# Kernel optimization log

Measured on AMD Instinct MI355X. Metric: run time of the kernel, lower is better.

The kernel has to match this reference:

```python
import jax, jax.numpy as jnp
import numpy as np

N_EMBD = 1024
N_HEAD = 16

def setup_inputs() -> dict:
    key = jax.random.key(0)
    k1, k2, k3 = jax.random.split(key, 3)
    x = jax.random.normal(k1, (2, 2048, N_EMBD), dtype=jnp.float32)
    # torch Linear(n, 3n): y = x @ W_attn (we store transposed weight directly)
    w_attn = jax.random.normal(k2, (N_EMBD, 3 * N_EMBD), dtype=jnp.float32) * 0.02
    w_proj = jax.random.normal(k3, (N_EMBD, N_EMBD), dtype=jnp.float32) * 0.02
    return {"x": x, "w_attn": w_attn, "w_proj": w_proj}

def reference(x, w_attn, w_proj):
    B, S, E = x.shape
    H = N_HEAD
    D = E // H
    qkv = x @ w_attn  # [B, S, 3E]
    q, k, v = jnp.split(qkv, 3, axis=-1)
    # [B, H, S, D]
    q = q.reshape(B, S, H, D).transpose(0, 2, 1, 3)
    k = k.reshape(B, S, H, D).transpose(0, 2, 1, 3)
    v = v.reshape(B, S, H, D).transpose(0, 2, 1, 3)
    scale = 1.0 / jnp.sqrt(jnp.asarray(D, dtype=x.dtype))
    a = jnp.einsum('bhqd,bhkd->bhqk', q, k) * scale  # [B, H, S, S]
    causal = jnp.tril(jnp.ones((S, S), dtype=bool))
    a = jnp.where(causal, a, -jnp.inf)
    a = jax.nn.softmax(a, axis=-1)
    y = jnp.einsum('bhqk,bhkd->bhqd', a, v)  # [B, H, S, D]
    y = y.transpose(0, 2, 1, 3).reshape(B, S, E)
    return y @ w_proj
```

## Files before the change

kernel.cpp:

```cpp
#include <hip/hip_runtime.h>

#define DEVI __device__ __forceinline__

typedef short bf16x8 __attribute__((ext_vector_type(8)));
typedef float f32x4 __attribute__((ext_vector_type(4)));
typedef unsigned short u16;
typedef unsigned int u32;

static constexpr int Bn = 2, S = 2048, E = 1024, H = 16, D = 64;
static constexpr int Mrows = Bn * S;
static constexpr int N_QKV = 3 * E;

DEVI u16 f2b(float f) {
  union { float f; u32 u; } c; c.f = f;
  return (u16)((c.u + 0x7FFFu + ((c.u >> 16) & 1u)) >> 16);
}

DEVI bf16x8 ld8(const u16* p) {
  union { uint4 u; bf16x8 v; } c;
  c.u = *reinterpret_cast<const uint4*>(p);
  return c.v;
}

#define MFMA(a, b, c) __builtin_amdgcn_mfma_f32_16x16x32_bf16(a, b, c, 0, 0, 0)

#define G2L16(gptr, lptr) \
  __builtin_amdgcn_global_load_lds((const __attribute__((address_space(1))) void*)(gptr), \
                                   (__attribute__((address_space(3))) void*)(lptr), 16, 0, 0)

__global__ void conv_bf16(const float* __restrict__ in, u16* __restrict__ out, int n4) {
  int i = blockIdx.x * blockDim.x + threadIdx.x;
  if (i < n4) {
    float4 f = reinterpret_cast<const float4*>(in)[i];
    ushort4 u;
    u.x = f2b(f.x); u.y = f2b(f.y); u.z = f2b(f.z); u.w = f2b(f.w);
    reinterpret_cast<ushort4*>(out)[i] = u;
  }
}

__global__ void transpose_bf16(const float* __restrict__ in, u16* __restrict__ out, int R, int C) {
  __shared__ float t[32][33];
  int bx = blockIdx.x * 32;
  int by = blockIdx.y * 32;
  int tx = threadIdx.x, ty = threadIdx.y;
#pragma unroll
  for (int k = 0; k < 32; k += 8)
    t[ty + k][tx] = in[(size_t)(by + ty + k) * C + bx + tx];
  __syncthreads();
#pragma unroll
  for (int k = 0; k < 32; k += 8)
    out[(size_t)(bx + ty + k) * R + by + tx] = f2b(t[tx][ty + k]);
}

__global__ __launch_bounds__(256) void gemm_qkv(const u16* __restrict__ A, const u16* __restrict__ BT,
                                                u16* __restrict__ Qb, u16* __restrict__ Kb,
                                                u16* __restrict__ VbT) {
  constexpr int K = 1024, BK = 64;
  __shared__ __align__(16) u16 As[128 * BK];
  __shared__ __align__(16) u16 Bs[128 * BK];
  int tid = threadIdx.x;
  int w = tid >> 6, lane = tid & 63, quad = lane >> 4, l15 = lane & 15;
  int m0 = blockIdx.x * 128, n0 = blockIdx.y * 128;
  int mw = (w >> 1) * 64, nw = (w & 1) * 64;
  const u16* Ab = A + (size_t)m0 * K;
  const u16* Bb = BT + (size_t)n0 * K;
  f32x4 acc[4][4] = {};
  for (int k0 = 0; k0 < K; k0 += BK) {
#pragma unroll
    for (int j = 0; j < 4; j++) {
      int L = j * 256 + tid;
      int row = L >> 3, cg = (L & 7) ^ (row & 7);
      G2L16(Ab + (size_t)row * K + k0 + cg * 8, (char*)As + L * 16);
    }
#pragma unroll
    for (int j = 0; j < 4; j++) {
      int L = j * 256 + tid;
      int row = L >> 3, cg = (L & 7) ^ (row & 7);
      G2L16(Bb + (size_t)row * K + k0 + cg * 8, (char*)Bs + L * 16);
    }
    __syncthreads();
#pragma unroll
    for (int kk = 0; kk < 2; kk++) {
      int sg = ((kk << 2) | quad) ^ (l15 & 7);
      bf16x8 a[4], b[4];
#pragma unroll
      for (int i = 0; i < 4; i++) a[i] = ld8(&As[(mw + i * 16 + l15) * BK + sg * 8]);
#pragma unroll
      for (int i = 0; i < 4; i++) b[i] = ld8(&Bs[(nw + i * 16 + l15) * BK + sg * 8]);
#pragma unroll
      for (int mb = 0; mb < 4; mb++)
#pragma unroll
        for (int nb = 0; nb < 4; nb++)
          acc[mb][nb] = MFMA(a[mb], b[nb], acc[mb][nb]);
    }
    __syncthreads();
  }
#pragma unroll
  for (int mb = 0; mb < 4; mb++) {
    int m = m0 + mw + mb * 16 + quad * 4;
    int b = m >> 11, s = m & 2047;
#pragma unroll
    for (int nb = 0; nb < 4; nb++) {
      int n = n0 + nw + nb * 16 + l15;
      int sec = n >> 10, e = n & 1023, h = e >> 6, d = e & 63;
      int bh = b * H + h;
      if (sec == 0) {
#pragma unroll
        for (int r = 0; r < 4; r++)
          Qb[((size_t)bh * S + s + r) * D + d] = f2b(acc[mb][nb][r] * 0.125f);
      } else if (sec == 1) {
#pragma unroll
        for (int r = 0; r < 4; r++)
          Kb[((size_t)bh * S + s + r) * D + d] = f2b(acc[mb][nb][r]);
      } else {
        ushort4 v;
        v.x = f2b(acc[mb][nb][0]); v.y = f2b(acc[mb][nb][1]);
        v.z = f2b(acc[mb][nb][2]); v.w = f2b(acc[mb][nb][3]);
        *reinterpret_cast<ushort4*>(VbT + ((size_t)bh * D + d) * S + s) = v;
      }
    }
  }
}

__global__ __launch_bounds__(256, 3) void attn(const u16* __restrict__ Qb, const u16* __restrict__ Kb,
                                               const u16* __restrict__ VbT, u16* __restrict__ Yb) {
  __shared__ __align__(16) u16 Ks[128 * 64];
  __shared__ __align__(16) u16 Vs[64 * 128];
  __shared__ __align__(16) u32 Ps[4][16 * 68];
  int w = threadIdx.x >> 6, lane = threadIdx.x & 63, quad = lane >> 4, l15 = lane & 15;
  int bh = blockIdx.x & 31, p = blockIdx.x >> 5;
  int b = bh >> 4, h = bh & 15;
  int qtA = 31 - p, qtB = p;
  int ncA = (qtA + 2) >> 1, ncB = (qtB + 2) >> 1;

  const u16* Kbh = Kb + (size_t)bh * S * D;
  const u16* Vbh = VbT + (size_t)bh * D * S;
  u32* myP = &Ps[w][0];
  const u16* myP16 = (const u16*)myP;
  int prow = l15 * 68 + quad * 2;

  int qbA = qtA * 64 + w * 16, qbB = qtB * 64 + w * 16;
  int kmaxA = qbA + 16, kmaxB = qbB + 16;
  const u16* QpA = Qb + ((size_t)bh * S + qbA + l15) * D + quad * 8;
  const u16* QpB = Qb + ((size_t)bh * S + qbB + l15) * D + quad * 8;
  bf16x8 bqA0 = ld8(QpA), bqA1 = ld8(QpA + 32);
  bf16x8 bqB0 = ld8(QpB), bqB1 = ld8(QpB + 32);

  float lA = 0.f, lB = 0.f;
  f32x4 oA[4] = {}, oB[4] = {};
  int kbase = 0;

  auto process = [&](int q_base, int kmaxW, bf16x8 bq0, bf16x8 bq1, f32x4* o, float& lpart) {
#pragma unroll
    for (int mb = 0; mb < 8; mb++) {
      int kb = kbase + mb * 16;
      u32 pa = 0, pb = 0;
      if (kb < kmaxW) {
        int row = mb * 16 + l15;
        bf16x8 ak0 = ld8(&Ks[row * 64 + ((quad ^ (row & 7)) * 8)]);
        bf16x8 ak1 = ld8(&Ks[row * 64 + (((quad + 4) ^ (row & 7)) * 8)]);
        f32x4 z = {};
        z = MFMA(ak0, bq0, z);
        z = MFMA(ak1, bq1, z);
        if (kb == q_base) {
#pragma unroll
          for (int r = 0; r < 4; r++)
            if (quad * 4 + r > l15) z[r] = -1e30f;
        }
        float p0 = __expf(z[0]), p1 = __expf(z[1]);
        float p2 = __expf(z[2]), p3 = __expf(z[3]);
        lpart += (p0 + p1) + (p2 + p3);
        pa = (u32)f2b(p0) | ((u32)f2b(p1) << 16);
        pb = (u32)f2b(p2) | ((u32)f2b(p3) << 16);
      }
      uint2 pw; pw.x = pa; pw.y = pb;
      *reinterpret_cast<uint2*>(&myP[prow + mb * 8]) = pw;
    }
#pragma unroll
    for (int ch = 0; ch < 4; ch++) {
      if (kbase + ch * 32 < kmaxW) {
        bf16x8 bp = ld8(myP16 + l15 * 136 + ch * 32 + quad * 8);
#pragma unroll
        for (int dd = 0; dd < 4; dd++) {
          int rv = dd * 16 + l15;
          bf16x8 av = ld8(&Vs[rv * 128 + (((ch * 4 + quad) ^ (rv & 15)) * 8)]);
          o[dd] = MFMA(av, bp, o[dd]);
        }
      }
    }
  };

  for (int c = 0; c < ncA; c++) {
    kbase = c * 128;
    __syncthreads();
    const u16* Kg = Kbh + (size_t)kbase * D;
#pragma unroll
    for (int j = 0; j < 4; j++) {
      int L = (w * 4 + j) * 64 + lane;
      int row = L >> 3, cg = (L & 7) ^ (row & 7);
      G2L16(Kg + (size_t)row * 64 + cg * 8, (char*)Ks + L * 16);
    }
    const u16* Vg = Vbh + kbase;
#pragma unroll
    for (int j = 0; j < 4; j++) {
      int L = (w * 4 + j) * 64 + lane;
      int row = L >> 4, cg = (L & 15) ^ (row & 15);
      G2L16(Vg + (size_t)row * S + cg * 8, (char*)Vs + L * 16);
    }
    __syncthreads();

    process(qbA, kmaxA, bqA0, bqA1, oA, lA);
    if (c < ncB)
      process(qbB, kmaxB, bqB0, bqB1, oB, lB);
  }

  {
    float l = lA; l += __shfl_xor(l, 16); l += __shfl_xor(l, 32);
    float rinv = 1.0f / l;
    u16* Yp = Yb + ((size_t)b * S + qbA + l15) * E + h * 64 + quad * 4;
#pragma unroll
    for (int dd = 0; dd < 4; dd++) {
      ushort4 y;
      y.x = f2b(oA[dd][0] * rinv); y.y = f2b(oA[dd][1] * rinv);
      y.z = f2b(oA[dd][2] * rinv); y.w = f2b(oA[dd][3] * rinv);
      *reinterpret_cast<ushort4*>(Yp + dd * 16) = y;
    }
  }
  {
    float l = lB; l += __shfl_xor(l, 16); l += __shfl_xor(l, 32);
    float rinv = 1.0f / l;
    u16* Yp = Yb + ((size_t)b * S + qbB + l15) * E + h * 64 + quad * 4;
#pragma unroll
    for (int dd = 0; dd < 4; dd++) {
      ushort4 y;
      y.x = f2b(oB[dd][0] * rinv); y.y = f2b(oB[dd][1] * rinv);
      y.z = f2b(oB[dd][2] * rinv); y.w = f2b(oB[dd][3] * rinv);
      *reinterpret_cast<ushort4*>(Yp + dd * 16) = y;
    }
  }
}

__global__ __launch_bounds__(256) void gemm_proj(const u16* __restrict__ A, const u16* __restrict__ BT,
                                                 float* __restrict__ out) {
  constexpr int K = 1024, BK = 64;
  __shared__ __align__(16) u16 As[128 * BK];
  __shared__ __align__(16) u16 Bs[128 * BK];
  int tid = threadIdx.x;
  int w = tid >> 6, lane = tid & 63, quad = lane >> 4, l15 = lane & 15;
  int m0 = blockIdx.x * 128, n0 = blockIdx.y * 128;
  int mw = (w >> 1) * 64, nw = (w & 1) * 64;
  const u16* Ab = A + (size_t)m0 * K;
  const u16* Bb = BT + (size_t)n0 * K;
  f32x4 acc[4][4] = {};
  for (int k0 = 0; k0 < K; k0 += BK) {
#pragma unroll
    for (int j = 0; j < 4; j++) {
      int L = j * 256 + tid;
      int row = L >> 3, cg = (L & 7) ^ (row & 7);
      G2L16(Ab + (size_t)row * K + k0 + cg * 8, (char*)As + L * 16);
    }
#pragma unroll
    for (int j = 0; j < 4; j++) {
      int L = j * 256 + tid;
      int row = L >> 3, cg = (L & 7) ^ (row & 7);
      G2L16(Bb + (size_t)row * K + k0 + cg * 8, (char*)Bs + L * 16);
    }
    __syncthreads();
#pragma unroll
    for (int kk = 0; kk < 2; kk++) {
      int sg = ((kk << 2) | quad) ^ (l15 & 7);
      bf16x8 a[4], b[4];
#pragma unroll
      for (int i = 0; i < 4; i++) a[i] = ld8(&As[(mw + i * 16 + l15) * BK + sg * 8]);
#pragma unroll
      for (int i = 0; i < 4; i++) b[i] = ld8(&Bs[(nw + i * 16 + l15) * BK + sg * 8]);
#pragma unroll
      for (int mb = 0; mb < 4; mb++)
#pragma unroll
        for (int nb = 0; nb < 4; nb++)
          acc[mb][nb] = MFMA(a[mb], b[nb], acc[mb][nb]);
    }
    __syncthreads();
  }
#pragma unroll
  for (int mb = 0; mb < 4; mb++) {
    int m = m0 + mw + mb * 16 + quad * 4;
#pragma unroll
    for (int nb = 0; nb < 4; nb++) {
      int n = n0 + nw + nb * 16 + l15;
#pragma unroll
      for (int r = 0; r < 4; r++)
        out[(size_t)(m + r) * E + n] = acc[mb][nb][r];
    }
  }
}

extern "C" void kernel_launch(void* const* d_in, const int* in_sizes, int n_in,
                              void* d_out, int out_size, void* d_ws, size_t ws_size,
                              hipStream_t stream) {
  const float* x = (const float*)d_in[0];
  const float* w_attn = (const float*)d_in[1];
  const float* w_proj = (const float*)d_in[2];
  float* out = (float*)d_out;
  char* ws = (char*)d_ws;

  u16* xb   = (u16*)(ws);
  u16* wabT = (u16*)(ws + 8388608);
  u16* wpbT = (u16*)(ws + 14680064);
  u16* Qb   = (u16*)(ws + 16777216);
  u16* Kb   = (u16*)(ws + 25165824);
  u16* VbT  = (u16*)(ws + 33554432);
  u16* Yb   = (u16*)(ws + 41943040);

  conv_bf16<<<4096, 256, 0, stream>>>(x, xb, Mrows * E / 4);
  transpose_bf16<<<dim3(N_QKV / 32, E / 32), dim3(32, 8), 0, stream>>>(w_attn, wabT, E, N_QKV);
  transpose_bf16<<<dim3(E / 32, E / 32), dim3(32, 8), 0, stream>>>(w_proj, wpbT, E, E);
  gemm_qkv<<<dim3(Mrows / 128, N_QKV / 128), 256, 0, stream>>>(xb, wabT, Qb, Kb, VbT);
  attn<<<Bn * H * (S / 128), 256, 0, stream>>>(Qb, Kb, VbT, Yb);
  gemm_proj<<<dim3(Mrows / 128, E / 128), 256, 0, stream>>>(Yb, wpbT, out);
}
```

Baseline: 188.9 us.

## Register-prefetch next K tile in QKV and projection GEMMs

Both GEMM kernels now load the next K tile from global memory into registers while the MFMAs for the current tile run, then store those registers to LDS at the top of the next iteration. This replaces the direct global-to-LDS copies that stalled before each compute step, so global latency is meant to overlap with compute. The cost is higher register pressure, an extra register-to-LDS store pass, and one wasted wrap-around prefetch on the last iteration.

```diff
diff --git a/kernel.cpp b/kernel.cpp
--- a/kernel.cpp
+++ b/kernel.cpp
@@ -64,21 +64,36 @@
   int mw = (w >> 1) * 64, nw = (w & 1) * 64;
   const u16* Ab = A + (size_t)m0 * K;
   const u16* Bb = BT + (size_t)n0 * K;
+
+  size_t goff[4]; int loff[4];
+#pragma unroll
+  for (int j = 0; j < 4; j++) {
+    int L = j * 256 + tid;
+    int row = L >> 3, cg = (L & 7) ^ (row & 7);
+    goff[j] = (size_t)row * K + cg * 8;
+    loff[j] = L * 16;
+  }
+  uint4 ra[4], rb[4];
+#pragma unroll
+  for (int j = 0; j < 4; j++) {
+    ra[j] = *reinterpret_cast<const uint4*>(Ab + goff[j]);
+    rb[j] = *reinterpret_cast<const uint4*>(Bb + goff[j]);
+  }
   f32x4 acc[4][4] = {};
   for (int k0 = 0; k0 < K; k0 += BK) {
-#pragma unroll
-    for (int j = 0; j < 4; j++) {
-      int L = j * 256 + tid;
-      int row = L >> 3, cg = (L & 7) ^ (row & 7);
-      G2L16(Ab + (size_t)row * K + k0 + cg * 8, (char*)As + L * 16);
-    }
-#pragma unroll
-    for (int j = 0; j < 4; j++) {
-      int L = j * 256 + tid;
-      int row = L >> 3, cg = (L & 7) ^ (row & 7);
-      G2L16(Bb + (size_t)row * K + k0 + cg * 8, (char*)Bs + L * 16);
-    }
-    __syncthreads();
+    __syncthreads();
+#pragma unroll
+    for (int j = 0; j < 4; j++) {
+      *reinterpret_cast<uint4*>((char*)As + loff[j]) = ra[j];
+      *reinterpret_cast<uint4*>((char*)Bs + loff[j]) = rb[j];
+    }
+    __syncthreads();
+    int kn = (k0 + BK) & (K - 1);
+#pragma unroll
+    for (int j = 0; j < 4; j++) {
+      ra[j] = *reinterpret_cast<const uint4*>(Ab + goff[j] + kn);
+      rb[j] = *reinterpret_cast<const uint4*>(Bb + goff[j] + kn);
+    }
 #pragma unroll
     for (int kk = 0; kk < 2; kk++) {
       int sg = ((kk << 2) | quad) ^ (l15 & 7);
@@ -93,7 +108,6 @@
         for (int nb = 0; nb < 4; nb++)
           acc[mb][nb] = MFMA(a[mb], b[nb], acc[mb][nb]);
     }
-    __syncthreads();
   }
 #pragma unroll
   for (int mb = 0; mb < 4; mb++) {
@@ -251,21 +265,35 @@
   int mw = (w >> 1) * 64, nw = (w & 1) * 64;
   const u16* Ab = A + (size_t)m0 * K;
   const u16* Bb = BT + (size_t)n0 * K;
+  size_t goff[4]; int loff[4];
+#pragma unroll
+  for (int j = 0; j < 4; j++) {
+    int L = j * 256 + tid;
+    int row = L >> 3, cg = (L & 7) ^ (row & 7);
+    goff[j] = (size_t)row * K + cg * 8;
+    loff[j] = L * 16;
+  }
+  uint4 ra[4], rb[4];
+#pragma unroll
+  for (int j = 0; j < 4; j++) {
+    ra[j] = *reinterpret_cast<const uint4*>(Ab + goff[j]);
+    rb[j] = *reinterpret_cast<const uint4*>(Bb + goff[j]);
+  }
   f32x4 acc[4][4] = {};
   for (int k0 = 0; k0 < K; k0 += BK) {
-#pragma unroll
-    for (int j = 0; j < 4; j++) {
-      int L = j * 256 + tid;
-      int row = L >> 3, cg = (L & 7) ^ (row & 7);
-      G2L16(Ab + (size_t)row * K + k0 + cg * 8, (char*)As + L * 16);
-    }
-#pragma unroll
-    for (int j = 0; j < 4; j++) {
-      int L = j * 256 + tid;
-      int row = L >> 3, cg = (L & 7) ^ (row & 7);
-      G2L16(Bb + (size_t)row * K + k0 + cg * 8, (char*)Bs + L * 16);
-    }
-    __syncthreads();
+    __syncthreads();
+#pragma unroll
+    for (int j = 0; j < 4; j++) {
+      *reinterpret_cast<uint4*>((char*)As + loff[j]) = ra[j];
+      *reinterpret_cast<uint4*>((char*)Bs + loff[j]) = rb[j];
+    }
+    __syncthreads();
+    int kn = (k0 + BK) & (K - 1);
+#pragma unroll
+    for (int j = 0; j < 4; j++) {
+      ra[j] = *reinterpret_cast<const uint4*>(Ab + goff[j] + kn);
+      rb[j] = *reinterpret_cast<const uint4*>(Bb + goff[j] + kn);
+    }
 #pragma unroll
     for (int kk = 0; kk < 2; kk++) {
       int sg = ((kk << 2) | quad) ^ (l15 & 7);
@@ -280,7 +308,6 @@
         for (int nb = 0; nb < 4; nb++)
           acc[mb][nb] = MFMA(a[mb], b[nb], acc[mb][nb]);
     }
-    __syncthreads();
   }
 #pragma unroll
   for (int mb = 0; mb < 4; mb++) {
```

Measured after the change: 295.0 us. 1.56x slower.
